# Performance work log

Hardware: AMD Instinct MI355X
Metric: run time of the kernel (lower is better)

The kernel has to match this reference:

```python
import jax, jax.numpy as jnp
import numpy as np

N_NODES = 50000
N_EDGES = 800000
IN_FEAT = 128
N_CLASSES = 64
K_HOPS = 2


def setup_inputs() -> dict:
    key = jax.random.key(0)
    k1, k2, k3, k4 = jax.random.split(key, 4)
    x = jax.random.normal(k1, (N_NODES, IN_FEAT), dtype=jnp.float32)
    edge_index = jax.random.randint(k2, (2, N_EDGES), 0, N_NODES, dtype=jnp.int64)
    # Linear layer params (PyTorch-style Kaiming-uniform-ish scale)
    lim = 1.0 / np.sqrt(IN_FEAT)
    W = jax.random.uniform(k3, (N_CLASSES, IN_FEAT), jnp.float32, -lim, lim)
    b = jax.random.uniform(k4, (N_CLASSES,), jnp.float32, -lim, lim)
    return {"x": x, "edge_index": edge_index, "W": W, "b": b}


def _sg_propagate(x, edge_index, K):
    """K-hop GCN-normalized propagation with self-loops (SGConv)."""
    N = x.shape[0]
    loop = jnp.arange(N, dtype=edge_index.dtype)
    row = jnp.concatenate([edge_index[0], loop])  # source nodes
    col = jnp.concatenate([edge_index[1], loop])  # target nodes
    deg = jax.ops.segment_sum(jnp.ones_like(col, dtype=x.dtype), col, num_segments=N)
    dinv = jnp.where(deg > 0, jax.lax.rsqrt(deg), 0.0)
    norm = dinv[row] * dinv[col]  # [E+N]
    for _ in range(K):
        x = jax.ops.segment_sum(norm[:, None] * x[row], col, num_segments=N)
    return x


def reference(x, edge_index, W, b):
    h = _sg_propagate(x, edge_index, K_HOPS)  # [N, in_features]
    return h @ W.T + b  # [N, num_classes]
```

## Files before the change

### kernel.cpp

```cpp
#include <hip/hip_runtime.h>
#include <hip/hip_fp16.h>

#define N_NODES   50000
#define N_EDGES   800000
#define IN_FEAT   128
#define N_CLASSES 64
#define LDS_PAD   132

__global__ void count_rank_kernel(const int* __restrict__ col, int* __restrict__ cnt,
                                  int* __restrict__ rank, int e) {
    int i = blockIdx.x * blockDim.x + threadIdx.x;
    if (i < e) rank[i] = atomicAdd(&cnt[col[i]], 1);
}

__global__ __launch_bounds__(256) void block_sum_kernel(const int* __restrict__ cnt,
                                                        int* __restrict__ bsum, int n) {
    __shared__ int s[256];
    int t = threadIdx.x;
    int i = blockIdx.x * 256 + t;
    s[t] = (i < n) ? cnt[i] : 0;
    __syncthreads();
    for (int off = 128; off > 0; off >>= 1) {
        if (t < off) s[t] += s[t + off];
        __syncthreads();
    }
    if (t == 0) bsum[blockIdx.x] = s[0];
}

__global__ __launch_bounds__(256) void scan_bsum_kernel(int* __restrict__ bsum, int nb) {
    __shared__ int s[256];
    int t = threadIdx.x;
    s[t] = (t < nb) ? bsum[t] : 0;
    __syncthreads();
    for (int off = 1; off < 256; off <<= 1) {
        int add = (t >= off) ? s[t - off] : 0;
        __syncthreads();
        s[t] += add;
        __syncthreads();
    }
    if (t < nb) bsum[t] = s[t];
}

__global__ __launch_bounds__(256) void apply_scan_kernel(const int* __restrict__ cnt,
                                                         const int* __restrict__ bsum,
                                                         int* __restrict__ rowptr,
                                                         float* __restrict__ dinv, int n) {
    __shared__ int s[256];
    int b = blockIdx.x, t = threadIdx.x;
    int i = b * 256 + t;
    int v = (i < n) ? cnt[i] : 0;
    s[t] = v;
    __syncthreads();
    for (int off = 1; off < 256; off <<= 1) {
        int add = (t >= off) ? s[t - off] : 0;
        __syncthreads();
        s[t] += add;
        __syncthreads();
    }
    int boff = (b > 0) ? bsum[b - 1] : 0;
    if (i < n) {
        rowptr[i] = boff + s[t] - v;
        dinv[i]   = rsqrtf((float)(v + 1));
    }
    if (i == n - 1) rowptr[n] = boff + s[t];
}

__global__ void scatter_kernel(const int* __restrict__ row, const int* __restrict__ col,
                               const int* __restrict__ rank, const int* __restrict__ rowptr,
                               int* __restrict__ adj, int e) {
    int i = blockIdx.x * blockDim.x + threadIdx.x;
    if (i < e) adj[rowptr[col[i]] + rank[i]] = row[i];
}

__global__ __launch_bounds__(256) void gemm_kernel(const float* __restrict__ x,
                                                   const float* __restrict__ W,
                                                   const float* __restrict__ dinv,
                                                   __half* __restrict__ u, int n) {
    __shared__ float xs[64][LDS_PAD];
    __shared__ float ws[64][LDS_PAD];
    int t = threadIdx.x;
    int rowbase = blockIdx.x * 64;

    for (int i = t; i < 64 * 32; i += 256) {
        int r  = i >> 5;
        int kk = i & 31;
        *(float4*)(&ws[r][kk * 4]) = *(const float4*)(W + (size_t)r * IN_FEAT + kk * 4);
        int gr = rowbase + r;
        float4 v = make_float4(0.f, 0.f, 0.f, 0.f);
        if (gr < n) v = *(const float4*)(x + (size_t)gr * IN_FEAT + kk * 4);
        *(float4*)(&xs[r][kk * 4]) = v;
    }
    __syncthreads();

    int rg = t >> 4;
    int cg = t & 15;
    float acc[4][4] = {};

    for (int kk = 0; kk < 32; ++kk) {
        float4 a[4], bb[4];
#pragma unroll
        for (int i = 0; i < 4; ++i) a[i]  = *(float4*)(&xs[rg + 16 * i][kk * 4]);
#pragma unroll
        for (int j = 0; j < 4; ++j) bb[j] = *(float4*)(&ws[cg + 16 * j][kk * 4]);
#pragma unroll
        for (int i = 0; i < 4; ++i)
#pragma unroll
            for (int j = 0; j < 4; ++j)
                acc[i][j] += a[i].x * bb[j].x + a[i].y * bb[j].y +
                             a[i].z * bb[j].z + a[i].w * bb[j].w;
    }

#pragma unroll
    for (int i = 0; i < 4; ++i) {
        int gr = rowbase + rg + 16 * i;
        if (gr < n) {
            float d = dinv[gr];
#pragma unroll
            for (int j = 0; j < 4; ++j)
                u[(size_t)gr * N_CLASSES + cg + 16 * j] = __float2half(d * acc[i][j]);
        }
    }
}

__global__ __launch_bounds__(256) void hop_sum_kernel(const int* __restrict__ rowptr,
                                                      const int* __restrict__ adj,
                                                      const float* __restrict__ dinv,
                                                      const __half* __restrict__ yin,
                                                      __half* __restrict__ yout_h,
                                                      float* __restrict__ yout_f,
                                                      const float* __restrict__ bias,
                                                      int mode, int n) {
    int sub  = threadIdx.x >> 6;
    int lane = threadIdx.x & 63;
    int node = blockIdx.x * 4 + sub;
    if (node >= n) return;

    int s  = rowptr[node];
    int e2 = rowptr[node + 1];

    float acc = __half2float(yin[(size_t)node * N_CLASSES + lane]);
    int k = s;
    for (; k + 7 < e2; k += 8) {
        float v0 = __half2float(yin[(size_t)adj[k + 0] * N_CLASSES + lane]);
        float v1 = __half2float(yin[(size_t)adj[k + 1] * N_CLASSES + lane]);
        float v2 = __half2float(yin[(size_t)adj[k + 2] * N_CLASSES + lane]);
        float v3 = __half2float(yin[(size_t)adj[k + 3] * N_CLASSES + lane]);
        float v4 = __half2float(yin[(size_t)adj[k + 4] * N_CLASSES + lane]);
        float v5 = __half2float(yin[(size_t)adj[k + 5] * N_CLASSES + lane]);
        float v6 = __half2float(yin[(size_t)adj[k + 6] * N_CLASSES + lane]);
        float v7 = __half2float(yin[(size_t)adj[k + 7] * N_CLASSES + lane]);
        acc += ((v0 + v1) + (v2 + v3)) + ((v4 + v5) + (v6 + v7));
    }
    for (; k < e2; ++k)
        acc += __half2float(yin[(size_t)adj[k] * N_CLASSES + lane]);

    float d = dinv[node];
    if (mode == 0) {
        yout_h[(size_t)node * N_CLASSES + lane] = __float2half(d * d * acc);
    } else {
        yout_f[(size_t)node * N_CLASSES + lane] = d * acc + bias[lane];
    }
}

extern "C" void kernel_launch(void* const* d_in, const int* in_sizes, int n_in,
                              void* d_out, int out_size, void* d_ws, size_t ws_size,
                              hipStream_t stream) {
    const float* x     = (const float*)d_in[0];
    const int*   edges = (const int*)d_in[1];
    const float* W     = (const float*)d_in[2];
    const float* b     = (const float*)d_in[3];
    float*       out   = (float*)d_out;

    const int* row = edges;
    const int* col = edges + N_EDGES;

    char* ws = (char*)d_ws;
    int*     cnt    = (int*)(ws + 0);
    int*     rowptr = (int*)(ws + 256 * 1024);
    float*   dinv   = (float*)(ws + 512 * 1024);
    int*     bsum   = (int*)(ws + 768 * 1024);
    int*     adj    = (int*)(ws + 1024 * 1024);
    int*     rank   = (int*)(ws + 4608 * 1024);
    __half*  u      = (__half*)(ws + 8 * 1024 * 1024);
    __half*  w1     = (__half*)(ws + 16 * 1024 * 1024);

    const int nblk = (N_NODES + 255) / 256;

    hipMemsetAsync(cnt, 0, N_NODES * sizeof(int), stream);
    count_rank_kernel<<<(N_EDGES + 255) / 256, 256, 0, stream>>>(col, cnt, rank, N_EDGES);
    block_sum_kernel<<<nblk, 256, 0, stream>>>(cnt, bsum, N_NODES);
    scan_bsum_kernel<<<1, 256, 0, stream>>>(bsum, nblk);
    apply_scan_kernel<<<nblk, 256, 0, stream>>>(cnt, bsum, rowptr, dinv, N_NODES);
    scatter_kernel<<<(N_EDGES + 255) / 256, 256, 0, stream>>>(row, col, rank, rowptr, adj, N_EDGES);

    gemm_kernel<<<(N_NODES + 63) / 64, 256, 0, stream>>>(x, W, dinv, u, N_NODES);

    hop_sum_kernel<<<(N_NODES + 3) / 4, 256, 0, stream>>>(rowptr, adj, dinv,
        u, w1, nullptr, nullptr, 0, N_NODES);
    hop_sum_kernel<<<(N_NODES + 3) / 4, 256, 0, stream>>>(rowptr, adj, dinv,
        w1, nullptr, out, b, 1, N_NODES);
}
```

Measured before the change: 158.7 us.

## Fuse CSR build stages into one cooperative kernel with grid syncs

Replaces the memset and five separate CSR construction kernels (count/rank, block sum, scan, apply scan, scatter) with a single cooperative kernel of 1024 blocks that uses grid-wide syncs between phases. This removes per-launch overhead and kernel boundaries for the small preprocessing steps. In exchange, grid.sync barriers cost time, grid-stride loops run with fewer threads than before, and cooperative launch requires all 1024 blocks to be co-resident.

```diff
diff --git a/kernel.cpp b/kernel.cpp
--- a/kernel.cpp
+++ b/kernel.cpp
@@ -1,5 +1,8 @@
 #include <hip/hip_runtime.h>
 #include <hip/hip_fp16.h>
+#include <hip/hip_cooperative_groups.h>
+
+namespace cg = cooperative_groups;
 
 #define N_NODES   50000
 #define N_EDGES   800000
@@ -7,69 +10,76 @@
 #define N_CLASSES 64
 #define LDS_PAD   132
 
-__global__ void count_rank_kernel(const int* __restrict__ col, int* __restrict__ cnt,
-                                  int* __restrict__ rank, int e) {
-    int i = blockIdx.x * blockDim.x + threadIdx.x;
-    if (i < e) rank[i] = atomicAdd(&cnt[col[i]], 1);
-}
-
-__global__ __launch_bounds__(256) void block_sum_kernel(const int* __restrict__ cnt,
-                                                        int* __restrict__ bsum, int n) {
-    __shared__ int s[256];
-    int t = threadIdx.x;
-    int i = blockIdx.x * 256 + t;
-    s[t] = (i < n) ? cnt[i] : 0;
-    __syncthreads();
-    for (int off = 128; off > 0; off >>= 1) {
-        if (t < off) s[t] += s[t + off];
-        __syncthreads();
-    }
-    if (t == 0) bsum[blockIdx.x] = s[0];
-}
-
-__global__ __launch_bounds__(256) void scan_bsum_kernel(int* __restrict__ bsum, int nb) {
-    __shared__ int s[256];
-    int t = threadIdx.x;
-    s[t] = (t < nb) ? bsum[t] : 0;
-    __syncthreads();
-    for (int off = 1; off < 256; off <<= 1) {
-        int add = (t >= off) ? s[t - off] : 0;
-        __syncthreads();
-        s[t] += add;
-        __syncthreads();
-    }
-    if (t < nb) bsum[t] = s[t];
-}
-
-__global__ __launch_bounds__(256) void apply_scan_kernel(const int* __restrict__ cnt,
-                                                         const int* __restrict__ bsum,
-                                                         int* __restrict__ rowptr,
-                                                         float* __restrict__ dinv, int n) {
-    __shared__ int s[256];
-    int b = blockIdx.x, t = threadIdx.x;
-    int i = b * 256 + t;
-    int v = (i < n) ? cnt[i] : 0;
-    s[t] = v;
-    __syncthreads();
-    for (int off = 1; off < 256; off <<= 1) {
-        int add = (t >= off) ? s[t - off] : 0;
-        __syncthreads();
-        s[t] += add;
-        __syncthreads();
-    }
-    int boff = (b > 0) ? bsum[b - 1] : 0;
-    if (i < n) {
-        rowptr[i] = boff + s[t] - v;
-        dinv[i]   = rsqrtf((float)(v + 1));
-    }
-    if (i == n - 1) rowptr[n] = boff + s[t];
-}
-
-__global__ void scatter_kernel(const int* __restrict__ row, const int* __restrict__ col,
-                               const int* __restrict__ rank, const int* __restrict__ rowptr,
-                               int* __restrict__ adj, int e) {
-    int i = blockIdx.x * blockDim.x + threadIdx.x;
-    if (i < e) adj[rowptr[col[i]] + rank[i]] = row[i];
+__global__ __launch_bounds__(256) void csr_build_kernel(const int* __restrict__ col,
+                                                        const int* __restrict__ row,
+                                                        int* __restrict__ cnt,
+                                                        int* __restrict__ rank,
+                                                        int* __restrict__ rowptr,
+                                                        float* __restrict__ dinv,
+                                                        int* __restrict__ adj,
+                                                        int* __restrict__ bsum) {
+    cg::grid_group grid = cg::this_grid();
+    __shared__ int sbuf[256];
+    const int t   = threadIdx.x;
+    const int tid = blockIdx.x * blockDim.x + t;
+    const int nth = gridDim.x * blockDim.x;
+    const int nch = (N_NODES + 255) / 256;
+
+    for (int i = tid; i < N_NODES; i += nth) cnt[i] = 0;
+    grid.sync();
+
+    for (int i = tid; i < N_EDGES; i += nth) rank[i] = atomicAdd(&cnt[col[i]], 1);
+    grid.sync();
+
+    for (int cb = blockIdx.x; cb < nch; cb += gridDim.x) {
+        int i = cb * 256 + t;
+        sbuf[t] = (i < N_NODES) ? cnt[i] : 0;
+        __syncthreads();
+        for (int off = 128; off > 0; off >>= 1) {
+            if (t < off) sbuf[t] += sbuf[t + off];
+            __syncthreads();
+        }
+        if (t == 0) bsum[cb] = sbuf[0];
+        __syncthreads();
+    }
+    grid.sync();
+
+    if (blockIdx.x == 0) {
+        sbuf[t] = (t < nch) ? bsum[t] : 0;
+        __syncthreads();
+        for (int off = 1; off < 256; off <<= 1) {
+            int add = (t >= off) ? sbuf[t - off] : 0;
+            __syncthreads();
+            sbuf[t] += add;
+            __syncthreads();
+        }
+        if (t < nch) bsum[t] = sbuf[t];
+    }
+    grid.sync();
+
+    for (int cb = blockIdx.x; cb < nch; cb += gridDim.x) {
+        int i = cb * 256 + t;
+        int v = (i < N_NODES) ? cnt[i] : 0;
+        sbuf[t] = v;
+        __syncthreads();
+        for (int off = 1; off < 256; off <<= 1) {
+            int add = (t >= off) ? sbuf[t - off] : 0;
+            __syncthreads();
+            sbuf[t] += add;
+            __syncthreads();
+        }
+        int boff = (cb > 0) ? bsum[cb - 1] : 0;
+        if (i < N_NODES) {
+            rowptr[i] = boff + sbuf[t] - v;
+            dinv[i]   = rsqrtf((float)(v + 1));
+        }
+        if (i == N_NODES - 1) rowptr[N_NODES] = boff + sbuf[t];
+        __syncthreads();
+    }
+    grid.sync();
+
+    for (int i = tid; i < N_EDGES; i += nth)
+        adj[rowptr[col[i]] + rank[i]] = row[i];
 }
 
 __global__ __launch_bounds__(256) void gemm_kernel(const float* __restrict__ x,
@@ -93,7 +103,7 @@
     __syncthreads();
 
     int rg = t >> 4;
-    int cg = t & 15;
+    int cg2 = t & 15;
     float acc[4][4] = {};
 
     for (int kk = 0; kk < 32; ++kk) {
@@ -101,7 +111,7 @@
 #pragma unroll
         for (int i = 0; i < 4; ++i) a[i]  = *(float4*)(&xs[rg + 16 * i][kk * 4]);
 #pragma unroll
-        for (int j = 0; j < 4; ++j) bb[j] = *(float4*)(&ws[cg + 16 * j][kk * 4]);
+        for (int j = 0; j < 4; ++j) bb[j] = *(float4*)(&ws[cg2 + 16 * j][kk * 4]);
 #pragma unroll
         for (int i = 0; i < 4; ++i)
 #pragma unroll
@@ -117,7 +127,7 @@
             float d = dinv[gr];
 #pragma unroll
             for (int j = 0; j < 4; ++j)
-                u[(size_t)gr * N_CLASSES + cg + 16 * j] = __float2half(d * acc[i][j]);
+                u[(size_t)gr * N_CLASSES + cg2 + 16 * j] = __float2half(d * acc[i][j]);
         }
     }
 }
@@ -184,14 +194,12 @@
     __half*  u      = (__half*)(ws + 8 * 1024 * 1024);
     __half*  w1     = (__half*)(ws + 16 * 1024 * 1024);
 
-    const int nblk = (N_NODES + 255) / 256;
-
-    hipMemsetAsync(cnt, 0, N_NODES * sizeof(int), stream);
-    count_rank_kernel<<<(N_EDGES + 255) / 256, 256, 0, stream>>>(col, cnt, rank, N_EDGES);
-    block_sum_kernel<<<nblk, 256, 0, stream>>>(cnt, bsum, N_NODES);
-    scan_bsum_kernel<<<1, 256, 0, stream>>>(bsum, nblk);
-    apply_scan_kernel<<<nblk, 256, 0, stream>>>(cnt, bsum, rowptr, dinv, N_NODES);
-    scatter_kernel<<<(N_EDGES + 255) / 256, 256, 0, stream>>>(row, col, rank, rowptr, adj, N_EDGES);
+    {
+        void* args[] = { (void*)&col, (void*)&row, (void*)&cnt, (void*)&rank,
+                         (void*)&rowptr, (void*)&dinv, (void*)&adj, (void*)&bsum };
+        hipLaunchCooperativeKernel((const void*)csr_build_kernel,
+                                   dim3(1024), dim3(256), args, 0, stream);
+    }
 
     gemm_kernel<<<(N_NODES + 63) / 64, 256, 0, stream>>>(x, W, dinv, u, N_NODES);
 
```

Result: slower. 628.4 us (+296.0%).
